# Optimization experiments

Measured on AMD Instinct MI355X. Metric: run time of the kernel, lower is better.

Reference implementation:

```python
import jax, jax.numpy as jnp
import numpy as np

B, H, W, K, PAD = 1024, 28, 28, 3, 1


def conv3x3(x, w, b):
    out = jax.lax.conv_general_dilated(x, w, (1, 1), ((PAD, PAD), (PAD, PAD)),
                                       dimension_numbers=('NCHW', 'OIHW', 'NCHW'))
    return out + b[None, :, None, None]


def deform_conv2d(x, offset, w, b):
    # torchvision deform_conv2d semantics, stride=1, pad=1, dilation=1, groups=1
    Bn, Cin, Hh, Ww = x.shape
    Cout = w.shape[0]
    KK = K * K
    off = offset.reshape(Bn, KK, 2, Hh, Ww)
    dy, dx = off[:, :, 0], off[:, :, 1]                      # [B,KK,H,W]
    ky, kx = jnp.meshgrid(jnp.arange(K, dtype=x.dtype), jnp.arange(K, dtype=x.dtype), indexing='ij')
    py = dy + (jnp.arange(Hh, dtype=x.dtype) - PAD)[None, None, :, None] + ky.reshape(KK)[None, :, None, None]
    px = dx + (jnp.arange(Ww, dtype=x.dtype) - PAD)[None, None, None, :] + kx.reshape(KK)[None, :, None, None]
    y0 = jnp.floor(py); x0 = jnp.floor(px)
    wy1 = py - y0; wy0 = 1.0 - wy1
    wx1 = px - x0; wx0 = 1.0 - wx1
    xf = x.reshape(Bn, Cin, Hh * Ww)

    def gather(yi, xi):
        valid = (yi >= 0) & (yi < Hh) & (xi >= 0) & (xi < Ww)
        yc = jnp.clip(yi, 0, Hh - 1).astype(jnp.int32)
        xc = jnp.clip(xi, 0, Ww - 1).astype(jnp.int32)
        idx = (yc * Ww + xc).reshape(Bn, -1)                 # [B, KK*H*W]
        g = jnp.take_along_axis(xf, jnp.broadcast_to(idx[:, None, :], (Bn, Cin, idx.shape[1])), axis=2)
        return g.reshape(Bn, Cin, KK, Hh, Ww) * valid.astype(x.dtype)[:, None]

    sampled = (gather(y0, x0) * (wy0 * wx0)[:, None]
               + gather(y0, x0 + 1) * (wy0 * wx1)[:, None]
               + gather(y0 + 1, x0) * (wy1 * wx0)[:, None]
               + gather(y0 + 1, x0 + 1) * (wy1 * wx1)[:, None])  # [B,Cin,KK,H,W]
    out = jnp.einsum('bkhw,ok->bohw', sampled.reshape(Bn, Cin * KK, Hh, Ww),
                     w.reshape(Cout, Cin * KK))
    return out + b[None, :, None, None]


def adaptive_avg_pool_14(x):
    Bn, C, Hh, Ww = x.shape
    f = Hh // 14
    return x.reshape(Bn, C, 14, f, 14, f).mean(axis=(3, 5))


def setup_inputs() -> dict:
    key = jax.random.key(0)
    ks = jax.random.split(key, 14)
    d = {}
    d['x'] = jax.random.normal(ks[0], (B, 1, H, W), dtype=jnp.float32)
    # offset conv 1: Conv2d(1, 18, 3, pad=1)
    d['ow1'] = jax.random.normal(ks[1], (18, 1, 3, 3), dtype=jnp.float32) * 0.1
    d['ob1'] = jnp.zeros((18,), jnp.float32)
    d['w1'] = jax.random.normal(ks[2], (32, 1, 3, 3), dtype=jnp.float32) * 0.01
    d['b1'] = jnp.zeros((32,), jnp.float32)
    # offset conv 2: Conv2d(32, 18, 3, pad=1)
    d['ow2'] = jax.random.normal(ks[3], (18, 32, 3, 3), dtype=jnp.float32) * 0.05
    d['ob2'] = jnp.zeros((18,), jnp.float32)
    d['w2'] = jax.random.normal(ks[4], (64, 32, 3, 3), dtype=jnp.float32) * 0.01
    d['b2'] = jnp.zeros((64,), jnp.float32)
    d['fw1'] = jax.random.normal(ks[5], (128, 64 * 14 * 14), dtype=jnp.float32) * 0.01
    d['fb1'] = jnp.zeros((128,), jnp.float32)
    d['fw2'] = jax.random.normal(ks[6], (10, 128), dtype=jnp.float32) * 0.05
    d['fb2'] = jnp.zeros((10,), jnp.float32)
    return d


def reference(x, ow1, ob1, w1, b1, ow2, ob2, w2, b2, fw1, fb1, fw2, fb2):
    # block1 + relu + pool 28->14
    h = deform_conv2d(x, conv3x3(x, ow1, ob1), w1, b1)
    h = adaptive_avg_pool_14(jax.nn.relu(h))
    # block2 + relu + pool 14->14 (identity)
    h = deform_conv2d(h, conv3x3(h, ow2, ob2), w2, b2)
    h = adaptive_avg_pool_14(jax.nn.relu(h))
    h = h.reshape(h.shape[0], -1)
    # classifier (ExcitationDropout is identity in eval mode)
    h = jax.nn.relu(h @ fw1.T + fb1)
    return h @ fw2.T + fb2
```

## Files before the change

### kernel.cpp

```cpp
#include <hip/hip_runtime.h>

#define NB 1024
#define TOTAL1 (NB*196)
#define SPS 200

#define WS_H1   0
#define WS_H2   6422528
#define WS_PART 19267584
#define WS_OFF2 WS_PART
#define WS_W1T  23461888
#define WS_OW1T 23462176
#define WS_W2T  23462338
#define WS_OW2T 23480770

__global__ __launch_bounds__(256) void prep(const float* __restrict__ w1,
                                            const float* __restrict__ ow1,
                                            const float* __restrict__ w2,
                                            const float* __restrict__ ow2,
                                            float* __restrict__ ws) {
  int i = blockIdx.x * 256 + threadIdx.x;
  if (i < 288)   { int co = i / 9,  kk = i % 9;   ws[WS_W1T  + kk * 32 + co] = w1[i]; }
  if (i < 162)   { int c  = i / 9,  j  = i % 9;   ws[WS_OW1T + j  * 18 + c ] = ow1[i]; }
  if (i < 18432) { int co = i / 288, k = i % 288; ws[WS_W2T  + k  * 64 + co] = w2[i]; }
  if (i < 5184)  { int c  = i / 288, k = i % 288; ws[WS_OW2T + k  * 18 + c ] = ow2[i]; }
}

__global__ __launch_bounds__(256, 2) void stage1(const float* __restrict__ x,
                                                 const float* __restrict__ ob1,
                                                 const float* __restrict__ b1,
                                                 const float* __restrict__ ws,
                                                 float* __restrict__ h1) {
  __shared__ float ximg[3 * 784];
  const float* __restrict__ w1t  = ws + WS_W1T;
  const float* __restrict__ ow1t = ws + WS_OW1T;
  int tid = threadIdx.x;
  int g0 = blockIdx.x * 256;
  int bfirst = g0 / 196;
  for (int idx = tid; idx < 3 * 784; idx += 256) {
    int img = idx / 784;
    int b = bfirst + img;
    ximg[idx] = (b < NB) ? x[b * 784 + (idx - img * 784)] : 0.f;
  }
  __syncthreads();
  int g = g0 + tid;
  if (g >= TOTAL1) return;
  int b = g / 196, p = g - b * 196;
  const float* im = ximg + (b - bfirst) * 784;
  int oy = p / 14, ox = p - (p / 14) * 14;

  float pooled[32];
#pragma unroll
  for (int co = 0; co < 32; ++co) pooled[co] = 0.f;

  for (int sub = 0; sub < 4; ++sub) {
    int y  = 2 * oy + (sub >> 1);
    int ix = 2 * ox + (sub & 1);
    float patch[9];
#pragma unroll
    for (int j = 0; j < 9; ++j) {
      int yy = y + j / 3 - 1, xc = ix + j % 3 - 1;
      bool ok = (yy >= 0) & (yy < 28) & (xc >= 0) & (xc < 28);
      patch[j] = ok ? im[yy * 28 + xc] : 0.f;
    }
    float off[18];
#pragma unroll
    for (int c = 0; c < 18; ++c) off[c] = ob1[c];
#pragma unroll
    for (int j = 0; j < 9; ++j) {
      float v = patch[j];
#pragma unroll
      for (int c = 0; c < 18; ++c) off[c] = fmaf(v, ow1t[j * 18 + c], off[c]);
    }
    float a[32];
#pragma unroll
    for (int co = 0; co < 32; ++co) a[co] = b1[co];
#pragma unroll
    for (int kk = 0; kk < 9; ++kk) {
      float py = (float)(y - 1 + kk / 3) + off[2 * kk];
      float px = (float)(ix - 1 + kk % 3) + off[2 * kk + 1];
      float y0f = floorf(py), x0f = floorf(px);
      float wy1 = py - y0f, wx1 = px - x0f;
      float wy0 = 1.f - wy1, wx0 = 1.f - wx1;
      int y0 = (int)y0f, x0 = (int)x0f;
      int y1 = y0 + 1, x1 = x0 + 1;
      bool vy0 = (y0 >= 0) & (y0 < 28), vy1 = (y1 >= 0) & (y1 < 28);
      bool vx0 = (x0 >= 0) & (x0 < 28), vx1 = (x1 >= 0) & (x1 < 28);
      float W00 = (vy0 & vx0) ? wy0 * wx0 : 0.f;
      float W01 = (vy0 & vx1) ? wy0 * wx1 : 0.f;
      float W10 = (vy1 & vx0) ? wy1 * wx0 : 0.f;
      float W11 = (vy1 & vx1) ? wy1 * wx1 : 0.f;
      int yc0 = min(max(y0, 0), 27), yc1 = min(max(y1, 0), 27);
      int xc0 = min(max(x0, 0), 27), xc1 = min(max(x1, 0), 27);
      float s = im[yc0 * 28 + xc0] * W00 + im[yc0 * 28 + xc1] * W01 +
                im[yc1 * 28 + xc0] * W10 + im[yc1 * 28 + xc1] * W11;
#pragma unroll
      for (int co = 0; co < 32; ++co) a[co] = fmaf(s, w1t[kk * 32 + co], a[co]);
    }
#pragma unroll
    for (int co = 0; co < 32; ++co) pooled[co] += fmaxf(a[co], 0.f);
  }
#pragma unroll
  for (int co = 0; co < 32; ++co) h1[b * 6272 + co * 196 + p] = pooled[co] * 0.25f;
}

__global__ __launch_bounds__(256, 4) void offconv(const float* __restrict__ h1,
                                                  const float* __restrict__ ob2,
                                                  const float* __restrict__ ws,
                                                  float* __restrict__ off2) {
  __shared__ float imgT[196 * 32];
  __shared__ float Sbuf[16 * SPS + 8];
  const float* __restrict__ ow2t = ws + WS_OW2T;
  int tid = threadIdx.x;
  int b = blockIdx.x;

  for (int e = tid; e < 6272; e += 256) {
    int ci = e / 196, p = e - ci * 196;
    imgT[p * 32 + ((ci + 4 * p) & 31)] = h1[b * 6272 + e];
  }
  if (tid < 64) Sbuf[(tid >> 2) * SPS + 196 + (tid & 3)] = 0.f;
  if (tid < 8)  Sbuf[16 * SPS + tid] = 0.f;

  int pp = tid;
  int spy = pp / 14, spx = pp - (pp / 14) * 14;
  int oc  = tid % 18;
  int opg = tid / 18;
  int op0 = opg * 16;
  bool oact = (tid < 234);
  float oacc[16];
#pragma unroll
  for (int i = 0; i < 16; ++i) oacc[i] = 0.f;

  for (int j = 0; j < 9; ++j) {
    for (int h = 0; h < 2; ++h) {
      __syncthreads();
      if (pp < 196) {
        int yy = spy + j / 3 - 1, xx = spx + j % 3 - 1;
        bool ok = (yy >= 0) & (yy < 14) & (xx >= 0) & (xx < 14);
        int idx = ok ? (yy * 14 + xx) : 0;
        const float* src = imgT + idx * 32;
        int rot = (4 * idx) & 31;
#pragma unroll
        for (int cg = 0; cg < 4; ++cg) {
          int cgg = h * 4 + cg;
          float4 v;
          if (ok) v = *(const float4*)(src + ((cgg * 4 + rot) & 31));
          else    v = make_float4(0.f, 0.f, 0.f, 0.f);
          Sbuf[(cg * 4 + 0) * SPS + pp] = v.x;
          Sbuf[(cg * 4 + 1) * SPS + pp] = v.y;
          Sbuf[(cg * 4 + 2) * SPS + pp] = v.z;
          Sbuf[(cg * 4 + 3) * SPS + pp] = v.w;
        }
      }
      __syncthreads();
      if (oact) {
        float wv[16];
#pragma unroll
        for (int l = 0; l < 16; ++l) wv[l] = ow2t[((h * 16 + l) * 9 + j) * 18 + oc];
        for (int l = 0; l < 16; ++l) {
          const float* srow = Sbuf + l * SPS + op0;
          float w = wv[l];
#pragma unroll
          for (int t = 0; t < 4; ++t) {
            float4 s = *(const float4*)(srow + 4 * t);
            oacc[4 * t + 0] = fmaf(w, s.x, oacc[4 * t + 0]);
            oacc[4 * t + 1] = fmaf(w, s.y, oacc[4 * t + 1]);
            oacc[4 * t + 2] = fmaf(w, s.z, oacc[4 * t + 2]);
            oacc[4 * t + 3] = fmaf(w, s.w, oacc[4 * t + 3]);
          }
        }
      }
    }
  }

  if (oact) {
    float bias = ob2[oc];
    float* dst = off2 + b * 3528 + oc * 196;
#pragma unroll
    for (int i = 0; i < 16; ++i)
      if (op0 + i < 196) dst[op0 + i] = oacc[i] + bias;
  }
}

__global__ __launch_bounds__(256, 4) void stage2(const float* __restrict__ h1,
                                                 const float* __restrict__ off2,
                                                 const float* __restrict__ b2,
                                                 const float* __restrict__ ws,
                                                 float* __restrict__ h2) {
  __shared__ float imgT[196 * 32];
  __shared__ float Sbuf2[2 * 1608];
  const float* __restrict__ w2t = ws + WS_W2T;
  int tid = threadIdx.x;
  int b = blockIdx.x;

  for (int e = tid; e < 6272; e += 256) {
    int ci = e / 196, p = e - ci * 196;
    imgT[p * 32 + ((ci + 4 * p) & 31)] = h1[b * 6272 + e];
  }

  int pp = tid;
  int spy = pp / 14, spx = pp - (pp / 14) * 14;
  bool samp = (pp < 196);
  const float* off_b = off2 + b * 3528;

  int cog = tid & 15, pg = tid >> 4;
  int co0 = cog * 4, p0 = pg * 16;
  bool gact = (pg < 13);
  float acc[4][16];
  {
    float4 bb = *(const float4*)(b2 + co0);
    float bj[4] = {bb.x, bb.y, bb.z, bb.w};
#pragma unroll
    for (int jj = 0; jj < 4; ++jj)
#pragma unroll
      for (int i = 0; i < 16; ++i) acc[jj][i] = bj[jj];
  }

  float W00 = 0.f, W01 = 0.f, W10 = 0.f, W11 = 0.f;
  int s00o = 0, s01o = 0, s10o = 0, s11o = 0;
  int r00 = 0, r01 = 0, r10 = 0, r11 = 0;
  float dyn = 0.f, dxn = 0.f;

  auto coeff = [&](int kkv) {
    float pyv = (float)(spy - 1 + kkv / 3) + dyn;
    float pxv = (float)(spx - 1 + kkv % 3) + dxn;
    float y0f = floorf(pyv), x0f = floorf(pxv);
    float wy1 = pyv - y0f, wx1 = pxv - x0f;
    float wy0 = 1.f - wy1, wx0 = 1.f - wx1;
    int y0 = (int)y0f, x0 = (int)x0f;
    int y1 = y0 + 1, x1 = x0 + 1;
    bool vy0 = (y0 >= 0) & (y0 < 14), vy1 = (y1 >= 0) & (y1 < 14);
    bool vx0 = (x0 >= 0) & (x0 < 14), vx1 = (x1 >= 0) & (x1 < 14);
    W00 = (vy0 & vx0) ? wy0 * wx0 : 0.f;
    W01 = (vy0 & vx1) ? wy0 * wx1 : 0.f;
    W10 = (vy1 & vx0) ? wy1 * wx0 : 0.f;
    W11 = (vy1 & vx1) ? wy1 * wx1 : 0.f;
    int yc0 = min(max(y0, 0), 13), yc1 = min(max(y1, 0), 13);
    int xc0 = min(max(x0, 0), 13), xc1 = min(max(x1, 0), 13);
    int i00 = yc0 * 14 + xc0, i01 = yc0 * 14 + xc1;
    int i10 = yc1 * 14 + xc0, i11 = yc1 * 14 + xc1;
    s00o = i00 * 32; r00 = (4 * i00) & 31;
    s01o = i01 * 32; r01 = (4 * i01) & 31;
    s10o = i10 * 32; r10 = (4 * i10) & 31;
    s11o = i11 * 32; r11 = (4 * i11) & 31;
  };

  auto sample = [&](int qn, int bufn) {
    float* dst = Sbuf2 + bufn * 1608 + pp;
#pragma unroll
    for (int cg = 0; cg < 2; ++cg) {
      int gq = qn * 2 + cg;
      float4 a0 = *(const float4*)(imgT + s00o + ((gq * 4 + r00) & 31));
      float4 a1 = *(const float4*)(imgT + s01o + ((gq * 4 + r01) & 31));
      float4 a2 = *(const float4*)(imgT + s10o + ((gq * 4 + r10) & 31));
      float4 a3 = *(const float4*)(imgT + s11o + ((gq * 4 + r11) & 31));
      dst[(cg * 4 + 0) * 200] = fmaf(W00, a0.x, fmaf(W01, a1.x, fmaf(W10, a2.x, W11 * a3.x)));
      dst[(cg * 4 + 1) * 200] = fmaf(W00, a0.y, fmaf(W01, a1.y, fmaf(W10, a2.y, W11 * a3.y)));
      dst[(cg * 4 + 2) * 200] = fmaf(W00, a0.z, fmaf(W01, a1.z, fmaf(W10, a2.z, W11 * a3.z)));
      dst[(cg * 4 + 3) * 200] = fmaf(W00, a0.w, fmaf(W01, a1.w, fmaf(W10, a2.w, W11 * a3.w)));
    }
  };

  if (samp) { dyn = off_b[pp]; dxn = off_b[196 + pp]; }
  __syncthreads();
  if (samp) { coeff(0); sample(0, 0); }
  __syncthreads();

  for (int kk = 0; kk < 9; ++kk) {
#pragma unroll
    for (int q = 0; q < 4; ++q) {
      if (samp && !((kk == 8) & (q == 3))) {
        if (q == 1 && kk < 8) {
          dyn = off_b[(2 * kk + 2) * 196 + pp];
          dxn = off_b[(2 * kk + 3) * 196 + pp];
        }
        if (q == 3) coeff(kk + 1);
        sample((q + 1) & 3, (q + 1) & 1);
      }
      if (gact) {
        const float* sb = Sbuf2 + (q & 1) * 1608 + p0;
        const float* wb = w2t + kk * 64 + co0;
#pragma unroll 2
        for (int l = 0; l < 8; ++l) {
          int ci = q * 8 + l;
          float4 w = *(const float4*)(wb + ci * 576);
          const float* srow = sb + l * 200;
          float4 s0 = *(const float4*)(srow);
          float4 s1 = *(const float4*)(srow + 4);
          float4 s2 = *(const float4*)(srow + 8);
          float4 s3 = *(const float4*)(srow + 12);
          float sv[16] = {s0.x, s0.y, s0.z, s0.w, s1.x, s1.y, s1.z, s1.w,
                          s2.x, s2.y, s2.z, s2.w, s3.x, s3.y, s3.z, s3.w};
          float wj[4] = {w.x, w.y, w.z, w.w};
#pragma unroll
          for (int jj = 0; jj < 4; ++jj)
#pragma unroll
            for (int i = 0; i < 16; ++i)
              acc[jj][i] = fmaf(wj[jj], sv[i], acc[jj][i]);
        }
      }
      __syncthreads();
    }
  }

  if (gact) {
    float* __restrict__ orow = h2 + b * 12544 + co0 * 196 + p0;
#pragma unroll
    for (int jj = 0; jj < 4; ++jj) {
#pragma unroll
      for (int t = 0; t < 4; ++t) {
        if (p0 + 4 * t < 196) {
          float4 v;
          v.x = fmaxf(acc[jj][4 * t + 0], 0.f);
          v.y = fmaxf(acc[jj][4 * t + 1], 0.f);
          v.z = fmaxf(acc[jj][4 * t + 2], 0.f);
          v.w = fmaxf(acc[jj][4 * t + 3], 0.f);
          *(float4*)(orow + jj * 196 + 4 * t) = v;
        }
      }
    }
  }
}

__global__ __launch_bounds__(256, 2) void fc1(const float* __restrict__ h2,
                                              const float* __restrict__ fw1,
                                              float* __restrict__ part) {
  __shared__ float a_s[56 * 72];
  __shared__ float b_s[56 * 132];
  int tid = threadIdx.x;
  int rb = (blockIdx.x & 15) * 64;
  int ks = blockIdx.x >> 4;
  int kbase = ks * 392;
  int c0 = (tid & 31) * 4;
  int r0 = (tid >> 5) * 8;

  float acc[8][4];
#pragma unroll
  for (int i = 0; i < 8; ++i)
#pragma unroll
    for (int j = 0; j < 4; ++j) acc[i][j] = 0.f;

  for (int ch = 0; ch < 7; ++ch) {
    int kb = kbase + ch * 56;
    __syncthreads();
#pragma unroll
    for (int t = 0; t < 14; ++t) {
      int idx = t * 256 + tid;
      int r = idx / 56, k = idx - r * 56;
      a_s[k * 72 + r] = h2[(rb + r) * 12544 + kb + k];
    }
#pragma unroll
    for (int t = 0; t < 28; ++t) {
      int idx = t * 256 + tid;
      int c = idx / 56, k = idx - c * 56;
      b_s[k * 132 + c] = fw1[c * 12544 + kb + k];
    }
    __syncthreads();
    for (int k = 0; k < 56; ++k) {
      float4 bv = *(const float4*)&b_s[k * 132 + c0];
      float4 av0 = *(const float4*)&a_s[k * 72 + r0];
      float4 av1 = *(const float4*)&a_s[k * 72 + r0 + 4];
      float av[8] = {av0.x, av0.y, av0.z, av0.w, av1.x, av1.y, av1.z, av1.w};
      float bj[4] = {bv.x, bv.y, bv.z, bv.w};
#pragma unroll
      for (int i = 0; i < 8; ++i)
#pragma unroll
        for (int j = 0; j < 4; ++j) acc[i][j] = fmaf(av[i], bj[j], acc[i][j]);
    }
  }
#pragma unroll
  for (int i = 0; i < 8; ++i) {
    int r = rb + r0 + i;
#pragma unroll
    for (int j = 0; j < 4; ++j)
      part[(ks * 1024 + r) * 128 + c0 + j] = acc[i][j];
  }
}

__global__ __launch_bounds__(128) void fcfinal(const float* __restrict__ part,
                                               const float* __restrict__ fb1,
                                               const float* __restrict__ fw2,
                                               const float* __restrict__ fb2,
                                               float* __restrict__ out) {
  __shared__ float tbuf[128];
  int b = blockIdx.x, c = threadIdx.x;
  float s = fb1[c];
  for (int ks = 0; ks < 32; ++ks) s += part[(ks * 1024 + b) * 128 + c];
  tbuf[c] = fmaxf(s, 0.f);
  __syncthreads();
  if (c < 10) {
    float v = fb2[c];
#pragma unroll
    for (int k = 0; k < 128; ++k) v = fmaf(tbuf[k], fw2[c * 128 + k], v);
    out[b * 10 + c] = v;
  }
}

extern "C" void kernel_launch(void* const* d_in, const int* in_sizes, int n_in,
                              void* d_out, int out_size, void* d_ws, size_t ws_size,
                              hipStream_t stream) {
  const float* x   = (const float*)d_in[0];
  const float* ow1 = (const float*)d_in[1];
  const float* ob1 = (const float*)d_in[2];
  const float* w1  = (const float*)d_in[3];
  const float* b1  = (const float*)d_in[4];
  const float* ow2 = (const float*)d_in[5];
  const float* ob2 = (const float*)d_in[6];
  const float* w2  = (const float*)d_in[7];
  const float* b2  = (const float*)d_in[8];
  const float* fw1 = (const float*)d_in[9];
  const float* fb1 = (const float*)d_in[10];
  const float* fw2 = (const float*)d_in[11];
  const float* fb2 = (const float*)d_in[12];
  float* ws  = (float*)d_ws;
  float* out = (float*)d_out;

  prep<<<72, 256, 0, stream>>>(w1, ow1, w2, ow2, ws);
  stage1<<<784, 256, 0, stream>>>(x, ob1, b1, ws, ws + WS_H1);
  offconv<<<NB, 256, 0, stream>>>(ws + WS_H1, ob2, ws, ws + WS_OFF2);
  stage2<<<NB, 256, 0, stream>>>(ws + WS_H1, ws + WS_OFF2, b2, ws, ws + WS_H2);
  fc1<<<512, 256, 0, stream>>>(ws + WS_H2, fw1, ws + WS_PART);
  fcfinal<<<1024, 128, 0, stream>>>(ws + WS_PART, fb1, fw2, fb2, out);
}
```

Baseline: 416.6 us.

## Fuse offset convolution into stage2 deform kernel, computing offsets per thread in registers

Removes the separate offconv kernel and computes the 18 offset channels for each output pixel directly inside stage2, reading from the already-loaded shared-memory image and keeping the results in registers. This drops a kernel launch, a second h1 load into shared memory, and the global write and reread of the offset tensor. In exchange, each sampling thread does the full 288x18 offset dot product serially while the GEMM threads wait at the barrier, and register pressure rises from the 18-element off array. The coeff selection over off[] uses unrolled compares so the array stays in registers.

```diff
diff --git a/kernel.cpp b/kernel.cpp
--- a/kernel.cpp
+++ b/kernel.cpp
@@ -2,12 +2,10 @@
 
 #define NB 1024
 #define TOTAL1 (NB*196)
-#define SPS 200
 
 #define WS_H1   0
 #define WS_H2   6422528
 #define WS_PART 19267584
-#define WS_OFF2 WS_PART
 #define WS_W1T  23461888
 #define WS_OW1T 23462176
 #define WS_W2T  23462338
@@ -103,92 +101,15 @@
   for (int co = 0; co < 32; ++co) h1[b * 6272 + co * 196 + p] = pooled[co] * 0.25f;
 }
 
-__global__ __launch_bounds__(256, 4) void offconv(const float* __restrict__ h1,
-                                                  const float* __restrict__ ob2,
-                                                  const float* __restrict__ ws,
-                                                  float* __restrict__ off2) {
-  __shared__ float imgT[196 * 32];
-  __shared__ float Sbuf[16 * SPS + 8];
-  const float* __restrict__ ow2t = ws + WS_OW2T;
-  int tid = threadIdx.x;
-  int b = blockIdx.x;
-
-  for (int e = tid; e < 6272; e += 256) {
-    int ci = e / 196, p = e - ci * 196;
-    imgT[p * 32 + ((ci + 4 * p) & 31)] = h1[b * 6272 + e];
-  }
-  if (tid < 64) Sbuf[(tid >> 2) * SPS + 196 + (tid & 3)] = 0.f;
-  if (tid < 8)  Sbuf[16 * SPS + tid] = 0.f;
-
-  int pp = tid;
-  int spy = pp / 14, spx = pp - (pp / 14) * 14;
-  int oc  = tid % 18;
-  int opg = tid / 18;
-  int op0 = opg * 16;
-  bool oact = (tid < 234);
-  float oacc[16];
-#pragma unroll
-  for (int i = 0; i < 16; ++i) oacc[i] = 0.f;
-
-  for (int j = 0; j < 9; ++j) {
-    for (int h = 0; h < 2; ++h) {
-      __syncthreads();
-      if (pp < 196) {
-        int yy = spy + j / 3 - 1, xx = spx + j % 3 - 1;
-        bool ok = (yy >= 0) & (yy < 14) & (xx >= 0) & (xx < 14);
-        int idx = ok ? (yy * 14 + xx) : 0;
-        const float* src = imgT + idx * 32;
-        int rot = (4 * idx) & 31;
-#pragma unroll
-        for (int cg = 0; cg < 4; ++cg) {
-          int cgg = h * 4 + cg;
-          float4 v;
-          if (ok) v = *(const float4*)(src + ((cgg * 4 + rot) & 31));
-          else    v = make_float4(0.f, 0.f, 0.f, 0.f);
-          Sbuf[(cg * 4 + 0) * SPS + pp] = v.x;
-          Sbuf[(cg * 4 + 1) * SPS + pp] = v.y;
-          Sbuf[(cg * 4 + 2) * SPS + pp] = v.z;
-          Sbuf[(cg * 4 + 3) * SPS + pp] = v.w;
-        }
-      }
-      __syncthreads();
-      if (oact) {
-        float wv[16];
-#pragma unroll
-        for (int l = 0; l < 16; ++l) wv[l] = ow2t[((h * 16 + l) * 9 + j) * 18 + oc];
-        for (int l = 0; l < 16; ++l) {
-          const float* srow = Sbuf + l * SPS + op0;
-          float w = wv[l];
-#pragma unroll
-          for (int t = 0; t < 4; ++t) {
-            float4 s = *(const float4*)(srow + 4 * t);
-            oacc[4 * t + 0] = fmaf(w, s.x, oacc[4 * t + 0]);
-            oacc[4 * t + 1] = fmaf(w, s.y, oacc[4 * t + 1]);
-            oacc[4 * t + 2] = fmaf(w, s.z, oacc[4 * t + 2]);
-            oacc[4 * t + 3] = fmaf(w, s.w, oacc[4 * t + 3]);
-          }
-        }
-      }
-    }
-  }
-
-  if (oact) {
-    float bias = ob2[oc];
-    float* dst = off2 + b * 3528 + oc * 196;
-#pragma unroll
-    for (int i = 0; i < 16; ++i)
-      if (op0 + i < 196) dst[op0 + i] = oacc[i] + bias;
-  }
-}
-
 __global__ __launch_bounds__(256, 4) void stage2(const float* __restrict__ h1,
-                                                 const float* __restrict__ off2,
+                                                 const float* __restrict__ ob2,
                                                  const float* __restrict__ b2,
                                                  const float* __restrict__ ws,
                                                  float* __restrict__ h2) {
   __shared__ float imgT[196 * 32];
   __shared__ float Sbuf2[2 * 1608];
-  const float* __restrict__ w2t = ws + WS_W2T;
+  const float* __restrict__ w2t  = ws + WS_W2T;
+  const float* __restrict__ ow2t = ws + WS_OW2T;
   int tid = threadIdx.x;
   int b = blockIdx.x;
 
@@ -200,7 +121,6 @@
   int pp = tid;
   int spy = pp / 14, spx = pp - (pp / 14) * 14;
   bool samp = (pp < 196);
-  const float* off_b = off2 + b * 3528;
 
   int cog = tid & 15, pg = tid >> 4;
   int co0 = cog * 4, p0 = pg * 16;
@@ -215,14 +135,47 @@
       for (int i = 0; i < 16; ++i) acc[jj][i] = bj[jj];
   }
 
+  __syncthreads();
+
+  float off[18];
+#pragma unroll
+  for (int c = 0; c < 18; ++c) off[c] = ob2[c];
+  if (samp) {
+    for (int j = 0; j < 9; ++j) {
+      int yy = spy + j / 3 - 1, xx = spx + j % 3 - 1;
+      bool ok = (yy >= 0) & (yy < 14) & (xx >= 0) & (xx < 14);
+      int nidx = ok ? (yy * 14 + xx) : 0;
+      const float* src = imgT + nidx * 32;
+      int rot = (4 * nidx) & 31;
+      for (int cq = 0; cq < 8; ++cq) {
+        float4 v;
+        if (ok) v = *(const float4*)(src + ((cq * 4 + rot) & 31));
+        else    v = make_float4(0.f, 0.f, 0.f, 0.f);
+        const float* wo0 = ow2t + ((cq * 4 + 0) * 9 + j) * 18;
+        const float* wo1 = ow2t + ((cq * 4 + 1) * 9 + j) * 18;
+        const float* wo2 = ow2t + ((cq * 4 + 2) * 9 + j) * 18;
+        const float* wo3 = ow2t + ((cq * 4 + 3) * 9 + j) * 18;
+#pragma unroll
+        for (int c = 0; c < 18; ++c) {
+          off[c] = fmaf(v.x, wo0[c], off[c]);
+          off[c] = fmaf(v.y, wo1[c], off[c]);
+          off[c] = fmaf(v.z, wo2[c], off[c]);
+          off[c] = fmaf(v.w, wo3[c], off[c]);
+        }
+      }
+    }
+  }
+
   float W00 = 0.f, W01 = 0.f, W10 = 0.f, W11 = 0.f;
   int s00o = 0, s01o = 0, s10o = 0, s11o = 0;
   int r00 = 0, r01 = 0, r10 = 0, r11 = 0;
-  float dyn = 0.f, dxn = 0.f;
 
   auto coeff = [&](int kkv) {
-    float pyv = (float)(spy - 1 + kkv / 3) + dyn;
-    float pxv = (float)(spx - 1 + kkv % 3) + dxn;
+    float dy = off[0], dx = off[1];
+#pragma unroll
+    for (int t = 1; t < 9; ++t) if (kkv == t) { dy = off[2 * t]; dx = off[2 * t + 1]; }
+    float pyv = (float)(spy - 1 + kkv / 3) + dy;
+    float pxv = (float)(spx - 1 + kkv % 3) + dx;
     float y0f = floorf(pyv), x0f = floorf(pxv);
     float wy1 = pyv - y0f, wx1 = pxv - x0f;
     float wy0 = 1.f - wy1, wx0 = 1.f - wx1;
@@ -260,8 +213,6 @@
     }
   };
 
-  if (samp) { dyn = off_b[pp]; dxn = off_b[196 + pp]; }
-  __syncthreads();
   if (samp) { coeff(0); sample(0, 0); }
   __syncthreads();
 
@@ -269,10 +220,6 @@
 #pragma unroll
     for (int q = 0; q < 4; ++q) {
       if (samp && !((kk == 8) & (q == 3))) {
-        if (q == 1 && kk < 8) {
-          dyn = off_b[(2 * kk + 2) * 196 + pp];
-          dxn = off_b[(2 * kk + 3) * 196 + pp];
-        }
         if (q == 3) coeff(kk + 1);
         sample((q + 1) & 3, (q + 1) & 1);
       }
@@ -416,8 +363,7 @@
 
   prep<<<72, 256, 0, stream>>>(w1, ow1, w2, ow2, ws);
   stage1<<<784, 256, 0, stream>>>(x, ob1, b1, ws, ws + WS_H1);
-  offconv<<<NB, 256, 0, stream>>>(ws + WS_H1, ob2, ws, ws + WS_OFF2);
-  stage2<<<NB, 256, 0, stream>>>(ws + WS_H1, ws + WS_OFF2, b2, ws, ws + WS_H2);
+  stage2<<<NB, 256, 0, stream>>>(ws + WS_H1, ob2, b2, ws, ws + WS_H2);
   fc1<<<512, 256, 0, stream>>>(ws + WS_H2, fw1, ws + WS_PART);
   fcfinal<<<1024, 128, 0, stream>>>(ws + WS_PART, fb1, fw2, fb2, out);
 }
```

After: 443.1 us. 6.4% more time.
